# Kernel optimization log

Measured on AMD Instinct MI355X. Metric: run time of the kernel, lower is better.

The kernel has to match this reference:

```python
import jax, jax.numpy as jnp
import numpy as np

FPS_NUM = 8
GROUP_NUM = 512
RADIUS = 0.2
H = 128
OUT = 128
NUM_LAYERS = 4
EPS = 1e-5
BIG = 1e10


def layernorm(x, g, b):
    m = x.mean(-1, keepdims=True)
    v = ((x - m) ** 2).mean(-1, keepdims=True)
    return (x - m) / jnp.sqrt(v + EPS) * g + b


def fps(xyz):
    # sequential farthest point sampling; deterministic start at index 0
    B, N, _ = xyz.shape

    def step(carry, _):
        distance, far = carry
        c = jnp.take_along_axis(xyz, far[:, None, None], axis=1)  # [B,1,3]
        d = jnp.sum((xyz - c) ** 2, axis=-1)                       # [B,N]
        distance = jnp.minimum(distance, d)
        return (distance, jnp.argmax(distance, axis=1)), far

    init = (jnp.full((B, N), BIG, xyz.dtype), jnp.zeros((B,), jnp.int32))
    _, cents = jax.lax.scan(step, init, None, length=FPS_NUM)
    return jnp.transpose(cents)  # [B, FPS_NUM]


def preprocess(xyz):
    B, N, _ = xyz.shape
    cents = fps(xyz)                                               # [B,K]
    cxyz = jnp.take_along_axis(xyz, cents[..., None], axis=1)      # [B,K,3]
    # ball query: pairwise sq-dist, mask outside radius, take GROUP_NUM nearest
    dist = jnp.sum((xyz[:, None, :, :] - cxyz[:, :, None, :]) ** 2, axis=-1)  # [B,K,N]
    dist = jnp.where(dist > RADIUS ** 2, BIG, dist)
    idx = jnp.argsort(dist, axis=-1)[:, :, :GROUP_NUM]             # [B,K,G]
    K = cents.shape[1]
    xyz_exp = jnp.broadcast_to(xyz[:, None, :, :], (B, K, N, 3))
    idx3 = jnp.broadcast_to(idx[..., None], (B, K, GROUP_NUM, 3))
    grouped = jnp.take_along_axis(xyz_exp, idx3, axis=2)           # [B,K,G,3]
    rel = grouped - cxyz[:, :, None, :]
    combined = jnp.concatenate([cxyz[:, :, None, :], rel], axis=2)  # [B,K,G+1,3]
    return combined, cxyz


def setup_inputs() -> dict:
    key = jax.random.key(0)
    ks = jax.random.split(key, 32)
    B, N = 32, 65536
    s = 0.05
    inp = {
        "x": jax.random.normal(ks[0], (B, N, 3), jnp.float32),
        "conv_in_w": jax.random.normal(ks[1], (H, 3), jnp.float32) * s,
        "conv_in_b": jnp.zeros((H,), jnp.float32),
        "layer_w": jax.random.normal(ks[2], (NUM_LAYERS, H, H), jnp.float32) * s,
        "layer_b": jnp.zeros((NUM_LAYERS, H), jnp.float32),
        "glayer_w": jax.random.normal(ks[3], (NUM_LAYERS, H, 2 * H), jnp.float32) * s,
        "glayer_b": jnp.zeros((NUM_LAYERS, H), jnp.float32),
        "conv_out_w": jax.random.normal(ks[4], (OUT, H * NUM_LAYERS), jnp.float32) * s,
        "conv_out_b": jnp.zeros((OUT,), jnp.float32),
        "mlp_w0": jax.random.normal(ks[5], (64, 3), jnp.float32) * s,
        "mlp_b0": jnp.zeros((64,), jnp.float32),
        "ln0_g": jnp.ones((64,), jnp.float32),
        "ln0_b": jnp.zeros((64,), jnp.float32),
        "mlp_w1": jax.random.normal(ks[6], (128, 64), jnp.float32) * s,
        "mlp_b1": jnp.zeros((128,), jnp.float32),
        "ln1_g": jnp.ones((128,), jnp.float32),
        "ln1_b": jnp.zeros((128,), jnp.float32),
        "mlp_w2": jax.random.normal(ks[7], (256, 128), jnp.float32) * s,
        "mlp_b2": jnp.zeros((256,), jnp.float32),
        "ln2_g": jnp.ones((256,), jnp.float32),
        "ln2_b": jnp.zeros((256,), jnp.float32),
        "fp_w": jax.random.normal(ks[8], (OUT, 256), jnp.float32) * s,
        "fp_b": jnp.zeros((OUT,), jnp.float32),
        "fp_ln_g": jnp.ones((OUT,), jnp.float32),
        "fp_ln_b": jnp.zeros((OUT,), jnp.float32),
    }
    return inp


def reference(x, conv_in_w, conv_in_b, layer_w, layer_b, glayer_w, glayer_b,
              conv_out_w, conv_out_b, mlp_w0, mlp_b0, ln0_g, ln0_b,
              mlp_w1, mlp_b1, ln1_g, ln1_b, mlp_w2, mlp_b2, ln2_g, ln2_b,
              fp_w, fp_b, fp_ln_g, fp_ln_b):
    combined, cx = preprocess(x)
    B, K, n, _ = combined.shape
    gp = combined.reshape(B * K, n, 3)
    # conv1x1 stack (LeakyReLU slope 0.0 == ReLU); layout [BK, n, C]
    y = jax.nn.relu(gp @ conv_in_w.T + conv_in_b)
    feats = []
    for i in range(NUM_LAYERS):
        y = jax.nn.relu(y @ layer_w[i].T + layer_b[i])
        yg = y.max(axis=1, keepdims=True)
        y = jnp.concatenate([y, jnp.broadcast_to(yg, y.shape)], axis=-1)
        y = jax.nn.relu(y @ glayer_w[i].T + glayer_b[i])
        feats.append(y)
    y = jnp.concatenate(feats, axis=-1)                 # [BK, n, H*L]
    y = (y @ conv_out_w.T + conv_out_b).max(axis=1)     # [BK, OUT]
    y_global = y.reshape(B, K, -1).max(axis=1)          # [B, OUT]

    c = jax.nn.relu(layernorm(cx @ mlp_w0.T + mlp_b0, ln0_g, ln0_b))
    c = jax.nn.relu(layernorm(c @ mlp_w1.T + mlp_b1, ln1_g, ln1_b))
    c = jax.nn.relu(layernorm(c @ mlp_w2.T + mlp_b2, ln2_g, ln2_b))
    c = c.max(axis=1)                                   # [B, 256]
    cf = layernorm(c @ fp_w.T + fp_b, fp_ln_g, fp_ln_b)  # [B, OUT]
    return (y_global, cf)
```

## Files before the change

kernel.cpp:

```cpp
#include <hip/hip_runtime.h>
#include <cstdint>
#include <cstddef>

#define N_PTS 65536
#define B_SZ 32
#define K_FPS 8
#define GRP 512
#define NP 513
#define HD 128
#define R2C 0.04f
#define BIGF 1e10f

typedef unsigned int u32;
typedef unsigned long long u64;
using bf8  = __attribute__((ext_vector_type(8))) short;
using f32x4 = __attribute__((ext_vector_type(4))) float;

__device__ __forceinline__ unsigned short f2bf(float f) {
  u32 u = __float_as_uint(f);
  u32 r = (u + 0x7FFFu + ((u >> 16) & 1u)) >> 16;
  return (unsigned short)r;
}
__device__ __forceinline__ float bf2f(unsigned short h) {
  return __uint_as_float(((u32)h) << 16);
}
__device__ __forceinline__ u32 xf(float v) {
  u32 u = __float_as_uint(v);
  return (u & 0x80000000u) ? ~u : (u | 0x80000000u);
}
__device__ __forceinline__ float xinv(u32 u) {
  return (u & 0x80000000u) ? __uint_as_float(u & 0x7FFFFFFFu) : __uint_as_float(~u);
}
__device__ __forceinline__ f32x4 mfma16(bf8 a, bf8 b, f32x4 c) {
  return __builtin_amdgcn_mfma_f32_16x16x32_bf16(a, b, c, 0, 0, 0);
}

__global__ void init_all_kernel(u32* __restrict__ slots32,
                                u32* __restrict__ tmaxU,
                                u32* __restrict__ goutU,
                                u32* __restrict__ cmaxU) {
  int i = blockIdx.x * blockDim.x + threadIdx.x;
  if (i < 448) slots32[i] = 0u;
  if (i < 4 * 256 * HD) tmaxU[i] = 0u;
  if (i < 256 * HD) goutU[i] = 0x00800000u;
  if (i < B_SZ * 256) cmaxU[i] = 0u;
}

template <int IT>
__global__ __launch_bounds__(256) void fps_step(const float* __restrict__ x,
                                                u64* __restrict__ slots) {
  int blk = blockIdx.x;
  int b = blk >> 6, s = blk & 63;
  int tid = threadIdx.x;
  const float* xb = x + (size_t)b * N_PTS * 3;
  __shared__ float cx[8], cy[8], cz[8];
  if (tid <= IT) {
    int ci = (tid == 0) ? 0 : (int)(0xFFFFFFFFu - (u32)slots[(tid - 1) * B_SZ + b]);
    cx[tid] = xb[ci * 3 + 0];
    cy[tid] = xb[ci * 3 + 1];
    cz[tid] = xb[ci * 3 + 2];
  }
  __syncthreads();
  float best = -1.0f; int bi = 0;
  int base = s * 1024;
#pragma unroll
  for (int j = 0; j < 4; ++j) {
    int i = base + j * 256 + tid;
    float px = xb[i * 3 + 0], py = xb[i * 3 + 1], pz = xb[i * 3 + 2];
    float d = BIGF;
#pragma unroll
    for (int c = 0; c <= IT; ++c) {
      float dx = px - cx[c], dy = py - cy[c], dz = pz - cz[c];
      d = fminf(d, dx * dx + dy * dy + dz * dz);
    }
    if (d > best) { best = d; bi = i; }
  }
  for (int off = 32; off > 0; off >>= 1) {
    float ov = __shfl_down(best, off);
    int oi = __shfl_down(bi, off);
    if (ov > best || (ov == best && oi < bi)) { best = ov; bi = oi; }
  }
  __shared__ float wv[4]; __shared__ int wi[4];
  if ((tid & 63) == 0) { wv[tid >> 6] = best; wi[tid >> 6] = bi; }
  __syncthreads();
  if (tid == 0) {
    float bv = wv[0]; int bx = wi[0];
    for (int k = 1; k < 4; ++k)
      if (wv[k] > bv || (wv[k] == bv && wi[k] < bx)) { bv = wv[k]; bx = wi[k]; }
    u64 key = ((u64)xf(bv) << 32) | (u64)(0xFFFFFFFFu - (u32)bx);
    atomicMax(&slots[IT * B_SZ + b], key);
  }
}

__global__ __launch_bounds__(1024) void ballq_kernel(const float* __restrict__ x,
                                                     const u64* __restrict__ slots,
                                                     float* __restrict__ cxyz,
                                                     float* __restrict__ grouped) {
  int i0 = blockIdx.x;
  int xcd = i0 & 7, j0 = i0 >> 3;
  int b = xcd + 8 * (j0 >> 3);
  int k = j0 & 7;
  int g = b * 8 + k;
  int tid = threadIdx.x;
  const float* xb = x + (size_t)b * N_PTS * 3;
  __shared__ int sPref[1024];
  __shared__ int s_in[GRP];
  __shared__ int s_out[GRP];
  __shared__ float sc[3];
  if (tid == 0) {
    int ci = (k == 0) ? 0 : (int)(0xFFFFFFFFu - (u32)slots[(k - 1) * B_SZ + b]);
    sc[0] = xb[ci * 3 + 0]; sc[1] = xb[ci * 3 + 1]; sc[2] = xb[ci * 3 + 2];
  }
  __syncthreads();
  float c0 = sc[0], c1 = sc[1], c2 = sc[2];
  int base = tid * 64;
  unsigned long long bm = 0ull;
  int cnt = 0;
  for (int j = 0; j < 64; ++j) {
    int i = base + j;
    float dx = xb[i * 3 + 0] - c0;
    float dy = xb[i * 3 + 1] - c1;
    float dz = xb[i * 3 + 2] - c2;
    float d = dx * dx + dy * dy + dz * dz;
    bool inr = !(d > R2C);
    if (inr) { bm |= (1ull << j); ++cnt; }
  }
  sPref[tid] = cnt;
  __syncthreads();
  for (int off = 1; off < 1024; off <<= 1) {
    int add = (tid >= off) ? sPref[tid - off] : 0;
    __syncthreads();
    sPref[tid] += add;
    __syncthreads();
  }
  int inc = sPref[tid];
  int exc = inc - cnt;
  int outExc = base - exc;
  {
    int ii = exc, oo = outExc;
    for (int j = 0; j < 64; ++j) {
      if ((bm >> j) & 1ull) { if (ii < GRP) s_in[ii] = base + j; ++ii; }
      else                  { if (oo < GRP) s_out[oo] = base + j; ++oo; }
    }
  }
  __syncthreads();
  int incnt = min(sPref[1023], GRP);
  if (tid == 0) {
    cxyz[g * 3 + 0] = c0; cxyz[g * 3 + 1] = c1; cxyz[g * 3 + 2] = c2;
    float* o0 = grouped + (size_t)g * NP * 3;
    o0[0] = c0; o0[1] = c1; o0[2] = c2;
  } else if (tid <= GRP) {
    int j = tid - 1;
    int src = (j < incnt) ? s_in[j] : s_out[j - incnt];
    float* o = grouped + ((size_t)g * NP + 1 + j) * 3;
    o[0] = xb[src * 3 + 0] - c0;
    o[1] = xb[src * 3 + 1] - c1;
    o[2] = xb[src * 3 + 2] - c2;
  }
}

__global__ void wprep_kernel(const float* __restrict__ layer_w,
                             const float* __restrict__ glayer_w,
                             const float* __restrict__ conv_out_w,
                             short* __restrict__ w1h, short* __restrict__ w1l,
                             short* __restrict__ w2h, short* __restrict__ w2l,
                             short* __restrict__ coh, short* __restrict__ col_) {
  int id = blockIdx.x * blockDim.x + threadIdx.x;
  float v; short *dh, *dl; size_t dpos;
  if (id < 65536) {
    int l = id >> 14, o = (id >> 7) & 127, k = id & 127;
    v = layer_w[(size_t)l * 16384 + o * 128 + k];
    dpos = (size_t)l * 16384 + o * 128 + (k ^ ((o & 7) << 3));
    dh = w1h; dl = w1l;
  } else if (id < 131072) {
    int t = id - 65536;
    int l = t >> 14, o = (t >> 7) & 127, k = t & 127;
    v = glayer_w[(size_t)l * 32768 + o * 256 + k];
    dpos = (size_t)l * 16384 + o * 128 + (k ^ ((o & 7) << 3));
    dh = w2h; dl = w2l;
  } else if (id < 196608) {
    int t = id - 131072;
    int o = t >> 9, k = t & 511;
    v = conv_out_w[(size_t)o * 512 + k];
    dpos = (size_t)o * 512 + (k ^ ((o & 7) << 3));
    dh = coh; dl = col_;
  } else return;
  unsigned short h = f2bf(v);
  dh[dpos] = (short)h;
  dl[dpos] = (short)f2bf(v - bf2f(h));
}

__global__ void conv_in_kernel(const float* __restrict__ gp,
                               const float* __restrict__ W,
                               const float* __restrict__ bias,
                               short* __restrict__ oh, short* __restrict__ ol,
                               int M, int Mp) {
  int idx = blockIdx.x * blockDim.x + threadIdx.x;
  if (idx >= Mp * HD) return;
  int r = idx >> 7, c = idx & 127;
  float v = 0.0f;
  if (r < M) {
    const float* p = gp + (size_t)r * 3;
    v = bias[c] + p[0] * W[c * 3 + 0] + p[1] * W[c * 3 + 1] + p[2] * W[c * 3 + 2];
    v = fmaxf(v, 0.0f);
  }
  unsigned short h = f2bf(v);
  size_t pos = (size_t)r * HD + (c ^ ((r & 7) << 3));
  oh[pos] = (short)h;
  ol[pos] = (short)f2bf(v - bf2f(h));
}

template <int MODE>
__global__ __launch_bounds__(256, 2) void mfgemm(
    const short* __restrict__ a0h, const short* __restrict__ a0l,
    const short* __restrict__ a1h, const short* __restrict__ a1l,
    const short* __restrict__ a2h, const short* __restrict__ a2l,
    const short* __restrict__ a3h, const short* __restrict__ a3l,
    const short* __restrict__ wh, const short* __restrict__ wl,
    int wRowShorts,
    const float* __restrict__ bias,
    short* __restrict__ oh, short* __restrict__ ol,
    u32* __restrict__ redU,
    int M) {
  __shared__ short lds[4][128][64];
  const int tid = threadIdx.x;
  const int lane = tid & 63, w = tid >> 6;
  const int wr = w >> 1, wc = w & 1;
  const int m0 = blockIdx.x * 128;
  const int wRB = wRowShorts * 2;

  f32x4 acc[4][4];
#pragma unroll
  for (int i = 0; i < 4; ++i)
#pragma unroll
    for (int j = 0; j < 4; ++j) acc[i][j] = (f32x4){0.f, 0.f, 0.f, 0.f};

  const int NH = (MODE == 2) ? 8 : 2;
  const short* ahp[4] = {a0h, a1h, a2h, a3h};
  const short* alp[4] = {a0l, a1l, a2l, a3l};

#pragma unroll
  for (int hf = 0; hf < NH; ++hf) {
    {
      const char* pAh = (const char*)ahp[hf >> 1] + (size_t)m0 * 256 + (hf & 1) * 128;
      const char* pAl = (const char*)alp[hf >> 1] + (size_t)m0 * 256 + (hf & 1) * 128;
      const char* pWh = (const char*)wh + hf * 128;
      const char* pWl = (const char*)wl + hf * 128;
#pragma unroll
      for (int i = 0; i < 16; ++i) {
        int c2 = i * 256 + tid;
        int plane = c2 >> 10;
        int idx = c2 & 1023;
        int row = idx >> 3, ch = idx & 7;
        const char* s = (plane == 0) ? pAh : (plane == 1) ? pAl
                       : (plane == 2) ? pWh : pWl;
        int rb = (plane < 2) ? 256 : wRB;
        const char* src = s + (size_t)row * rb + ch * 16;
        void* dst = (char*)lds + (size_t)c2 * 16;
        __builtin_amdgcn_global_load_lds(
            (const __attribute__((address_space(1))) u32*)src,
            (__attribute__((address_space(3))) u32*)dst, 16, 0, 0);
      }
    }
    __syncthreads();
#pragma unroll
    for (int kk = 0; kk < 2; ++kk) {
      int k0 = kk * 32 + (lane >> 4) * 8;
      bf8 afh[4], afl[4], bfh[4], bfl[4];
#pragma unroll
      for (int rt = 0; rt < 4; ++rt) {
        int row = wr * 64 + rt * 16 + (lane & 15);
        int kp = k0 ^ ((row & 7) << 3);
        afh[rt] = *(const bf8*)&lds[0][row][kp];
        afl[rt] = *(const bf8*)&lds[1][row][kp];
      }
#pragma unroll
      for (int ct = 0; ct < 4; ++ct) {
        int orow = wc * 64 + ct * 16 + (lane & 15);
        int kp = k0 ^ ((orow & 7) << 3);
        bfh[ct] = *(const bf8*)&lds[2][orow][kp];
        bfl[ct] = *(const bf8*)&lds[3][orow][kp];
      }
#pragma unroll
      for (int rt = 0; rt < 4; ++rt)
#pragma unroll
        for (int ct = 0; ct < 4; ++ct) {
          acc[rt][ct] = mfma16(afh[rt], bfh[ct], acc[rt][ct]);
          acc[rt][ct] = mfma16(afh[rt], bfl[ct], acc[rt][ct]);
          acc[rt][ct] = mfma16(afl[rt], bfh[ct], acc[rt][ct]);
        }
    }
    if (hf + 1 < NH) __syncthreads();
  }

#pragma unroll
  for (int ct = 0; ct < 4; ++ct) {
    int col = wc * 64 + ct * 16 + (lane & 15);
    int curGrp = -1;
    u32 curKey = 0;
#pragma unroll
    for (int rt = 0; rt < 4; ++rt) {
      int rbase = m0 + wr * 64 + rt * 16 + ((lane >> 4) << 2);
#pragma unroll
      for (int reg = 0; reg < 4; ++reg) {
        int row = rbase + reg;
        float v = acc[rt][ct][reg];
        if (MODE == 0) v += bias[col];
        if (MODE == 1) v += bias[(row / 513) * HD + col];
        if (MODE != 2) {
          v = fmaxf(v, 0.0f);
          unsigned short h = f2bf(v);
          unsigned short l2 = f2bf(v - bf2f(h));
          size_t pos = (size_t)row * HD + (col ^ ((row & 7) << 3));
          oh[pos] = (short)h;
          ol[pos] = (short)l2;
        }
        if (MODE == 0 || MODE == 2) {
          if (row < M) {
            int gg = row / 513;
            u32 key = xf(v);
            if (gg != curGrp) {
              if (curGrp >= 0) atomicMax(&redU[curGrp * HD + col], curKey);
              curGrp = gg; curKey = key;
            } else {
              curKey = max(curKey, key);
            }
          }
        }
      }
    }
    if ((MODE == 0 || MODE == 2) && curGrp >= 0)
      atomicMax(&redU[curGrp * HD + col], curKey);
  }
}

__global__ void gvec_kernel(const u32* __restrict__ tmaxU, const float* __restrict__ gw,
                            const float* __restrict__ gb, float* __restrict__ gvec) {
  int g = blockIdx.x, c = threadIdx.x;
  __shared__ float sm[HD];
  sm[c] = xinv(tmaxU[g * HD + c]);
  __syncthreads();
  const float* wr = gw + (size_t)c * (2 * HD) + HD;
  float s = gb[c];
  for (int j = 0; j < HD; ++j) s += sm[j] * wr[j];
  gvec[g * HD + c] = s;
}

__global__ void batchmax_kernel(const u32* __restrict__ goutU,
                                const float* __restrict__ bout,
                                float* __restrict__ out) {
  int b = blockIdx.x, c = threadIdx.x;
  float m = -3.4e38f;
  for (int k = 0; k < K_FPS; ++k) m = fmaxf(m, xinv(goutU[(size_t)(b * K_FPS + k) * HD + c]));
  out[b * HD + c] = m + bout[c];
}

__device__ __forceinline__ void block_ln(float* h, int n, const float* __restrict__ gam,
                                         const float* __restrict__ bet, float* red,
                                         int tid, bool relu) {
  float v = (tid < n) ? h[tid] : 0.0f;
  red[tid] = v;
  __syncthreads();
  for (int s = 128; s > 0; s >>= 1) { if (tid < s) red[tid] += red[tid + s]; __syncthreads(); }
  float mean = red[0] / n;
  __syncthreads();
  float d = (tid < n) ? (h[tid] - mean) : 0.0f;
  red[tid] = d * d;
  __syncthreads();
  for (int s = 128; s > 0; s >>= 1) { if (tid < s) red[tid] += red[tid + s]; __syncthreads(); }
  float var = red[0] / n;
  __syncthreads();
  if (tid < n) {
    float o = (h[tid] - mean) / sqrtf(var + 1e-5f) * gam[tid] + bet[tid];
    if (relu) o = fmaxf(o, 0.0f);
    h[tid] = o;
  }
  __syncthreads();
}

__global__ __launch_bounds__(256) void cpathA_kernel(const float* __restrict__ cxyz,
    const float* __restrict__ w0, const float* __restrict__ b0,
    const float* __restrict__ g0, const float* __restrict__ e0,
    const float* __restrict__ w1, const float* __restrict__ b1,
    const float* __restrict__ g1, const float* __restrict__ e1,
    const float* __restrict__ w2, const float* __restrict__ b2,
    const float* __restrict__ g2, const float* __restrict__ e2,
    u32* __restrict__ cmaxU) {
  int g = blockIdx.x, b = g >> 3, tid = threadIdx.x;
  __shared__ float h[256];
  __shared__ float hb[256];
  __shared__ float red[256];
  const float* cp = cxyz + (size_t)g * 3;
  float p0 = cp[0], p1 = cp[1], p2 = cp[2];
  if (tid < 64)
    h[tid] = b0[tid] + p0 * w0[tid * 3 + 0] + p1 * w0[tid * 3 + 1] + p2 * w0[tid * 3 + 2];
  __syncthreads();
  block_ln(h, 64, g0, e0, red, tid, true);
  if (tid < 128) {
    float s = b1[tid];
    const float* wr = w1 + (size_t)tid * 64;
    for (int j = 0; j < 64; ++j) s += h[j] * wr[j];
    hb[tid] = s;
  }
  __syncthreads();
  block_ln(hb, 128, g1, e1, red, tid, true);
  {
    float s = b2[tid];
    const float* wr = w2 + (size_t)tid * 128;
    for (int j = 0; j < 128; ++j) s += hb[j] * wr[j];
    __syncthreads();
    h[tid] = s;
  }
  __syncthreads();
  block_ln(h, 256, g2, e2, red, tid, true);
  atomicMax(&cmaxU[b * 256 + tid], xf(h[tid]));
}

__global__ __launch_bounds__(256) void cpathB_kernel(const u32* __restrict__ cmaxU,
    const float* __restrict__ fw, const float* __restrict__ fb,
    const float* __restrict__ fg, const float* __restrict__ fe,
    float* __restrict__ out) {
  int b = blockIdx.x, tid = threadIdx.x;
  __shared__ float cm[256];
  __shared__ float h[256];
  __shared__ float red[256];
  cm[tid] = xinv(cmaxU[b * 256 + tid]);
  __syncthreads();
  if (tid < 128) {
    float s = fb[tid];
    const float* wr = fw + (size_t)tid * 256;
    for (int j = 0; j < 256; ++j) s += cm[j] * wr[j];
    h[tid] = s;
  }
  __syncthreads();
  block_ln(h, 128, fg, fe, red, tid, false);
  if (tid < 128) out[b * HD + tid] = h[tid];
}

extern "C" void kernel_launch(void* const* d_in, const int* in_sizes, int n_in,
                              void* d_out, int out_size, void* d_ws, size_t ws_size,
                              hipStream_t stream) {
  (void)in_sizes; (void)n_in; (void)out_size;
  const float* x          = (const float*)d_in[0];
  const float* conv_in_w  = (const float*)d_in[1];
  const float* conv_in_b  = (const float*)d_in[2];
  const float* layer_w    = (const float*)d_in[3];
  const float* layer_b    = (const float*)d_in[4];
  const float* glayer_w   = (const float*)d_in[5];
  const float* glayer_b   = (const float*)d_in[6];
  const float* conv_out_w = (const float*)d_in[7];
  const float* conv_out_b = (const float*)d_in[8];
  const float* mlp_w0 = (const float*)d_in[9];
  const float* mlp_b0 = (const float*)d_in[10];
  const float* ln0_g  = (const float*)d_in[11];
  const float* ln0_b  = (const float*)d_in[12];
  const float* mlp_w1 = (const float*)d_in[13];
  const float* mlp_b1 = (const float*)d_in[14];
  const float* ln1_g  = (const float*)d_in[15];
  const float* ln1_b  = (const float*)d_in[16];
  const float* mlp_w2 = (const float*)d_in[17];
  const float* mlp_b2 = (const float*)d_in[18];
  const float* ln2_g  = (const float*)d_in[19];
  const float* ln2_b  = (const float*)d_in[20];
  const float* fp_w   = (const float*)d_in[21];
  const float* fp_b   = (const float*)d_in[22];
  const float* fp_ln_g = (const float*)d_in[23];
  const float* fp_ln_b = (const float*)d_in[24];

  char* ws = (char*)d_ws;
  size_t off = 0;
  auto carve = [&](size_t bytes) -> void* {
    void* p = ws + off;
    off += (bytes + 255) & ~(size_t)255;
    return p;
  };
  u64* slots   = (u64*)carve(7 * B_SZ * 8);
  float* cxyz  = (float*)carve(256 * 3 * 4);
  float* grouped = (float*)carve((size_t)256 * NP * 3 * 4);
  u32* goutU   = (u32*)carve(256 * HD * 4);
  u32* tmaxU   = (u32*)carve(4 * 256 * HD * 4);
  float* gvec  = (float*)carve(257 * HD * 4);
  u32* cmaxU   = (u32*)carve(B_SZ * 256 * 4);
  short* w1h = (short*)carve(4 * 16384 * 2);
  short* w1l = (short*)carve(4 * 16384 * 2);
  short* w2h = (short*)carve(4 * 16384 * 2);
  short* w2l = (short*)carve(4 * 16384 * 2);
  short* coh = (short*)carve(65536 * 2);
  short* col_ = (short*)carve(65536 * 2);
  size_t fixed = off;

  int C = 8;
  const int cands[5] = {128, 64, 32, 16, 8};
  for (int ci = 0; ci < 5; ++ci) {
    int Cc = cands[ci];
    size_t Mp = ((size_t)(513 * Cc + 127) / 128) * 128;
    size_t need = fixed + 12 * ((Mp * HD * 2 + 255) & ~(size_t)255) + 65536;
    if (need <= ws_size) { C = Cc; break; }
  }
  int Mp = (int)(((size_t)(513 * C + 127) / 128) * 128);
  size_t planeB = (size_t)Mp * HD * 2;
  short* y0h = (short*)carve(planeB); short* y0l = (short*)carve(planeB);
  short* th  = (short*)carve(planeB); short* tl  = (short*)carve(planeB);
  short* fh[4]; short* fl[4];
  for (int l = 0; l < 4; ++l) { fh[l] = (short*)carve(planeB); fl[l] = (short*)carve(planeB); }

  init_all_kernel<<<(4 * 256 * HD + 255) / 256, 256, 0, stream>>>(
      (u32*)slots, tmaxU, goutU, cmaxU);

  fps_step<0><<<2048, 256, 0, stream>>>(x, slots);
  fps_step<1><<<2048, 256, 0, stream>>>(x, slots);
  fps_step<2><<<2048, 256, 0, stream>>>(x, slots);
  fps_step<3><<<2048, 256, 0, stream>>>(x, slots);
  fps_step<4><<<2048, 256, 0, stream>>>(x, slots);
  fps_step<5><<<2048, 256, 0, stream>>>(x, slots);
  fps_step<6><<<2048, 256, 0, stream>>>(x, slots);

  ballq_kernel<<<256, 1024, 0, stream>>>(x, slots, cxyz, grouped);
  wprep_kernel<<<768, 256, 0, stream>>>(layer_w, glayer_w, conv_out_w,
                                        w1h, w1l, w2h, w2l, coh, col_);

  int M = C * 513;
  int nb = Mp / 128;
  for (int g0 = 0; g0 < 256; g0 += C) {
    conv_in_kernel<<<(Mp * HD + 255) / 256, 256, 0, stream>>>(
        grouped + (size_t)g0 * NP * 3, conv_in_w, conv_in_b, y0h, y0l, M, Mp);
    const short* inH = y0h; const short* inL = y0l;
    for (int l = 0; l < 4; ++l) {
      u32* tmaxL = tmaxU + (size_t)l * 256 * HD + (size_t)g0 * HD;
      mfgemm<0><<<nb, 256, 0, stream>>>(
          inH, inL, inH, inL, inH, inL, inH, inL,
          w1h + (size_t)l * 16384, w1l + (size_t)l * 16384, 128,
          layer_b + l * HD, th, tl, tmaxL, M);
      gvec_kernel<<<C, HD, 0, stream>>>(tmaxL, glayer_w + (size_t)l * HD * 2 * HD,
                                        glayer_b + l * HD, gvec);
      mfgemm<1><<<nb, 256, 0, stream>>>(
          th, tl, th, tl, th, tl, th, tl,
          w2h + (size_t)l * 16384, w2l + (size_t)l * 16384, 128,
          gvec, fh[l], fl[l], nullptr, M);
      inH = fh[l]; inL = fl[l];
    }
    mfgemm<2><<<nb, 256, 0, stream>>>(
        fh[0], fl[0], fh[1], fl[1], fh[2], fl[2], fh[3], fl[3],
        coh, col_, 512, nullptr, nullptr, nullptr, goutU + (size_t)g0 * HD, M);
  }
  batchmax_kernel<<<B_SZ, HD, 0, stream>>>(goutU, conv_out_b, (float*)d_out);
  cpathA_kernel<<<256, 256, 0, stream>>>(cxyz,
      mlp_w0, mlp_b0, ln0_g, ln0_b,
      mlp_w1, mlp_b1, ln1_g, ln1_b,
      mlp_w2, mlp_b2, ln2_g, ln2_b, cmaxU);
  cpathB_kernel<<<B_SZ, 256, 0, stream>>>(cmaxU, fp_w, fp_b, fp_ln_g, fp_ln_b,
                                          (float*)d_out + B_SZ * HD);
}
```

Before: 886.5 us.

## Fuse conv_in into first GEMM, halve GEMM tile rows, stage stores via LDS

Removes the separate conv_in kernel by computing the 3->128 input conv inside a new GEMM mode that writes the A tile straight into LDS. This drops the y0 buffers and one full write/read of the activation planes. The GEMM M-tile shrinks from 128 to 64 rows, with occupancy raised to 3 blocks per CU, and outputs are staged through LDS for coalesced 16-byte stores. The block-to-batch mapping in the FPS and ball-query kernels is also remapped for XCD locality. The smaller tile means less weight reuse per block, and the ballq remap changes which batch each block handles.

Result: faster. 779.2 us (-12.1%).

```diff
diff --git a/kernel.cpp b/kernel.cpp
--- a/kernel.cpp
+++ b/kernel.cpp
@@ -13,8 +13,10 @@
 
 typedef unsigned int u32;
 typedef unsigned long long u64;
-using bf8  = __attribute__((ext_vector_type(8))) short;
+using bf8   = __attribute__((ext_vector_type(8))) short;
+using s8v   = __attribute__((ext_vector_type(8))) short;
 using f32x4 = __attribute__((ext_vector_type(4))) float;
+using i32x4 = __attribute__((ext_vector_type(4))) int;
 
 __device__ __forceinline__ unsigned short f2bf(float f) {
   u32 u = __float_as_uint(f);
@@ -49,8 +51,8 @@
 template <int IT>
 __global__ __launch_bounds__(256) void fps_step(const float* __restrict__ x,
                                                 u64* __restrict__ slots) {
-  int blk = blockIdx.x;
-  int b = blk >> 6, s = blk & 63;
+  int p = (blockIdx.x & 7) * 256 + (blockIdx.x >> 3);
+  int b = p >> 6, s = p & 63;
   int tid = threadIdx.x;
   const float* xb = x + (size_t)b * N_PTS * 3;
   __shared__ float cx[8], cy[8], cz[8];
@@ -96,9 +98,9 @@
                                                      const u64* __restrict__ slots,
                                                      float* __restrict__ cxyz,
                                                      float* __restrict__ grouped) {
-  int i0 = blockIdx.x;
-  int xcd = i0 & 7, j0 = i0 >> 3;
-  int b = xcd + 8 * (j0 >> 3);
+  int blk = blockIdx.x;
+  int xcd = blk & 7, j0 = blk >> 3;
+  int b = xcd * 4 + (j0 >> 3);
   int k = j0 & 7;
   int g = b * 8 + k;
   int tid = threadIdx.x;
@@ -190,28 +192,8 @@
   dl[dpos] = (short)f2bf(v - bf2f(h));
 }
 
-__global__ void conv_in_kernel(const float* __restrict__ gp,
-                               const float* __restrict__ W,
-                               const float* __restrict__ bias,
-                               short* __restrict__ oh, short* __restrict__ ol,
-                               int M, int Mp) {
-  int idx = blockIdx.x * blockDim.x + threadIdx.x;
-  if (idx >= Mp * HD) return;
-  int r = idx >> 7, c = idx & 127;
-  float v = 0.0f;
-  if (r < M) {
-    const float* p = gp + (size_t)r * 3;
-    v = bias[c] + p[0] * W[c * 3 + 0] + p[1] * W[c * 3 + 1] + p[2] * W[c * 3 + 2];
-    v = fmaxf(v, 0.0f);
-  }
-  unsigned short h = f2bf(v);
-  size_t pos = (size_t)r * HD + (c ^ ((r & 7) << 3));
-  oh[pos] = (short)h;
-  ol[pos] = (short)f2bf(v - bf2f(h));
-}
-
 template <int MODE>
-__global__ __launch_bounds__(256, 2) void mfgemm(
+__global__ __launch_bounds__(256, 3) void mfgemm(
     const short* __restrict__ a0h, const short* __restrict__ a0l,
     const short* __restrict__ a1h, const short* __restrict__ a1l,
     const short* __restrict__ a2h, const short* __restrict__ a2l,
@@ -219,19 +201,21 @@
     const short* __restrict__ wh, const short* __restrict__ wl,
     int wRowShorts,
     const float* __restrict__ bias,
+    const float* __restrict__ cw, const float* __restrict__ cb,
+    const float* __restrict__ gp,
     short* __restrict__ oh, short* __restrict__ ol,
-    u32* __restrict__ redU,
-    int M) {
-  __shared__ short lds[4][128][64];
+    u32* __restrict__ redU, int M) {
+  __shared__ alignas(16) short ldsA[2][64][64];
+  __shared__ alignas(16) short ldsW[2][128][64];
   const int tid = threadIdx.x;
   const int lane = tid & 63, w = tid >> 6;
   const int wr = w >> 1, wc = w & 1;
-  const int m0 = blockIdx.x * 128;
+  const int m0 = blockIdx.x * 64;
   const int wRB = wRowShorts * 2;
 
-  f32x4 acc[4][4];
-#pragma unroll
-  for (int i = 0; i < 4; ++i)
+  f32x4 acc[2][4];
+#pragma unroll
+  for (int i = 0; i < 2; ++i)
 #pragma unroll
     for (int j = 0; j < 4; ++j) acc[i][j] = (f32x4){0.f, 0.f, 0.f, 0.f};
 
@@ -239,50 +223,91 @@
   const short* ahp[4] = {a0h, a1h, a2h, a3h};
   const short* alp[4] = {a0l, a1l, a2l, a3l};
 
-#pragma unroll
+  float gx = 0.f, gy = 0.f, gz = 0.f;
+  if (MODE == 3) {
+    int row = m0 + (tid >> 2);
+    if (row < M) { gx = gp[row * 3]; gy = gp[row * 3 + 1]; gz = gp[row * 3 + 2]; }
+  }
+
   for (int hf = 0; hf < NH; ++hf) {
-    {
-      const char* pAh = (const char*)ahp[hf >> 1] + (size_t)m0 * 256 + (hf & 1) * 128;
-      const char* pAl = (const char*)alp[hf >> 1] + (size_t)m0 * 256 + (hf & 1) * 128;
-      const char* pWh = (const char*)wh + hf * 128;
-      const char* pWl = (const char*)wl + hf * 128;
-#pragma unroll
-      for (int i = 0; i < 16; ++i) {
+    if (MODE == 3) {
+#pragma unroll
+      for (int i = 0; i < 8; ++i) {
         int c2 = i * 256 + tid;
-        int plane = c2 >> 10;
-        int idx = c2 & 1023;
+        int plane = c2 >> 10, idx = c2 & 1023;
         int row = idx >> 3, ch = idx & 7;
-        const char* s = (plane == 0) ? pAh : (plane == 1) ? pAl
-                       : (plane == 2) ? pWh : pWl;
-        int rb = (plane < 2) ? 256 : wRB;
-        const char* src = s + (size_t)row * rb + ch * 16;
-        void* dst = (char*)lds + (size_t)c2 * 16;
+        const char* s = plane ? (const char*)wl : (const char*)wh;
+        const char* src = s + (size_t)row * wRB + hf * 128 + ch * 16;
+        void* dst = (char*)ldsW[plane] + (size_t)idx * 16;
         __builtin_amdgcn_global_load_lds(
             (const __attribute__((address_space(1))) u32*)src,
             (__attribute__((address_space(3))) u32*)dst, 16, 0, 0);
       }
+      int r = tid >> 2, q = tid & 3;
+      bool real = (m0 + r) < M;
+#pragma unroll
+      for (int jj = 0; jj < 2; ++jj) {
+        short hbuf[8], lbuf[8];
+#pragma unroll
+        for (int j = 0; j < 8; ++j) {
+          int c = hf * 64 + q * 16 + jj * 8 + j;
+          float v = 0.f;
+          if (real)
+            v = fmaxf(cb[c] + gx * cw[c * 3] + gy * cw[c * 3 + 1] + gz * cw[c * 3 + 2], 0.f);
+          unsigned short hh = f2bf(v);
+          hbuf[j] = (short)hh;
+          lbuf[j] = (short)f2bf(v - bf2f(hh));
+        }
+        int pos = (q * 16 + jj * 8) ^ ((r & 7) << 3);
+        *(s8v*)&ldsA[0][r][pos] = *(const s8v*)hbuf;
+        *(s8v*)&ldsA[1][r][pos] = *(const s8v*)lbuf;
+      }
+    } else {
+#pragma unroll
+      for (int i = 0; i < 12; ++i) {
+        int c2 = i * 256 + tid;
+        const char* src;
+        void* dst;
+        if (c2 < 1024) {
+          int plane = c2 >> 9, idx = c2 & 511;
+          int row = idx >> 3, ch = idx & 7;
+          const char* s = plane ? (const char*)alp[hf >> 1] : (const char*)ahp[hf >> 1];
+          src = s + (size_t)(m0 + row) * 256 + (hf & 1) * 128 + ch * 16;
+          dst = (char*)ldsA[plane] + (size_t)idx * 16;
+        } else {
+          int t = c2 - 1024;
+          int plane = t >> 10, idx = t & 1023;
+          int row = idx >> 3, ch = idx & 7;
+          const char* s = plane ? (const char*)wl : (const char*)wh;
+          src = s + (size_t)row * wRB + hf * 128 + ch * 16;
+          dst = (char*)ldsW[plane] + (size_t)idx * 16;
+        }
+        __builtin_amdgcn_global_load_lds(
+            (const __attribute__((address_space(1))) u32*)src,
+            (__attribute__((address_space(3))) u32*)dst, 16, 0, 0);
+      }
     }
     __syncthreads();
 #pragma unroll
     for (int kk = 0; kk < 2; ++kk) {
       int k0 = kk * 32 + (lane >> 4) * 8;
-      bf8 afh[4], afl[4], bfh[4], bfl[4];
-#pragma unroll
-      for (int rt = 0; rt < 4; ++rt) {
-        int row = wr * 64 + rt * 16 + (lane & 15);
+      bf8 afh[2], afl[2], bfh[4], bfl[4];
+#pragma unroll
+      for (int rt = 0; rt < 2; ++rt) {
+        int row = wr * 32 + rt * 16 + (lane & 15);
         int kp = k0 ^ ((row & 7) << 3);
-        afh[rt] = *(const bf8*)&lds[0][row][kp];
-        afl[rt] = *(const bf8*)&lds[1][row][kp];
+        afh[rt] = *(const bf8*)&ldsA[0][row][kp];
+        afl[rt] = *(const bf8*)&ldsA[1][row][kp];
       }
 #pragma unroll
       for (int ct = 0; ct < 4; ++ct) {
         int orow = wc * 64 + ct * 16 + (lane & 15);
         int kp = k0 ^ ((orow & 7) << 3);
-        bfh[ct] = *(const bf8*)&lds[2][orow][kp];
-        bfl[ct] = *(const bf8*)&lds[3][orow][kp];
+        bfh[ct] = *(const bf8*)&ldsW[0][orow][kp];
+        bfl[ct] = *(const bf8*)&ldsW[1][orow][kp];
       }
 #pragma unroll
-      for (int rt = 0; rt < 4; ++rt)
+      for (int rt = 0; rt < 2; ++rt)
 #pragma unroll
         for (int ct = 0; ct < 4; ++ct) {
           acc[rt][ct] = mfma16(afh[rt], bfh[ct], acc[rt][ct]);
@@ -290,47 +315,59 @@
           acc[rt][ct] = mfma16(afl[rt], bfh[ct], acc[rt][ct]);
         }
     }
-    if (hf + 1 < NH) __syncthreads();
-  }
-
+    __syncthreads();
+  }
+
+  constexpr bool DO_STORE = (MODE != 2);
+  constexpr bool DO_RED   = (MODE != 1);
+  short* imgH = (short*)ldsA;
+  short* imgL = (short*)ldsW;
 #pragma unroll
   for (int ct = 0; ct < 4; ++ct) {
     int col = wc * 64 + ct * 16 + (lane & 15);
     int curGrp = -1;
     u32 curKey = 0;
 #pragma unroll
-    for (int rt = 0; rt < 4; ++rt) {
-      int rbase = m0 + wr * 64 + rt * 16 + ((lane >> 4) << 2);
+    for (int rt = 0; rt < 2; ++rt) {
+      int rb = wr * 32 + rt * 16 + ((lane >> 4) << 2);
 #pragma unroll
       for (int reg = 0; reg < 4; ++reg) {
-        int row = rbase + reg;
+        int lrow = rb + reg;
+        int row = m0 + lrow;
         float v = acc[rt][ct][reg];
-        if (MODE == 0) v += bias[col];
+        if (MODE == 0 || MODE == 3) v += bias[col];
         if (MODE == 1) v += bias[(row / 513) * HD + col];
-        if (MODE != 2) {
-          v = fmaxf(v, 0.0f);
-          unsigned short h = f2bf(v);
-          unsigned short l2 = f2bf(v - bf2f(h));
-          size_t pos = (size_t)row * HD + (col ^ ((row & 7) << 3));
-          oh[pos] = (short)h;
-          ol[pos] = (short)l2;
+        if (MODE != 2) v = fmaxf(v, 0.0f);
+        if (DO_STORE) {
+          unsigned short hh = f2bf(v);
+          int pos = lrow * 128 + (col ^ ((lrow & 7) << 3));
+          imgH[pos] = (short)hh;
+          imgL[pos] = (short)f2bf(v - bf2f(hh));
         }
-        if (MODE == 0 || MODE == 2) {
-          if (row < M) {
-            int gg = row / 513;
-            u32 key = xf(v);
-            if (gg != curGrp) {
-              if (curGrp >= 0) atomicMax(&redU[curGrp * HD + col], curKey);
-              curGrp = gg; curKey = key;
-            } else {
-              curKey = max(curKey, key);
-            }
+        if (DO_RED && row < M) {
+          int gg = row / 513;
+          u32 key = xf(v);
+          if (gg != curGrp) {
+            if (curGrp >= 0) atomicMax(&redU[curGrp * HD + col], curKey);
+            curGrp = gg; curKey = key;
+          } else {
+            curKey = max(curKey, key);
           }
         }
       }
     }
-    if ((MODE == 0 || MODE == 2) && curGrp >= 0)
-      atomicMax(&redU[curGrp * HD + col], curKey);
+    if (DO_RED && curGrp >= 0) atomicMax(&redU[curGrp * HD + col], curKey);
+  }
+  if (DO_STORE) {
+    __syncthreads();
+    char* dH = (char*)oh + (size_t)m0 * 256;
+    char* dL = (char*)ol + (size_t)m0 * 256;
+#pragma unroll
+    for (int i = 0; i < 4; ++i) {
+      int idx = i * 256 + tid;
+      *(i32x4*)(dH + (size_t)idx * 16) = *(const i32x4*)((const char*)imgH + (size_t)idx * 16);
+      *(i32x4*)(dL + (size_t)idx * 16) = *(const i32x4*)((const char*)imgL + (size_t)idx * 16);
+    }
   }
 }
 
@@ -493,14 +530,15 @@
   const int cands[5] = {128, 64, 32, 16, 8};
   for (int ci = 0; ci < 5; ++ci) {
     int Cc = cands[ci];
-    size_t Mp = ((size_t)(513 * Cc + 127) / 128) * 128;
-    size_t need = fixed + 12 * ((Mp * HD * 2 + 255) & ~(size_t)255) + 65536;
+    size_t Mp = ((size_t)(513 * Cc + 63) / 64) * 64;
+    size_t need = fixed + 10 * ((Mp * HD * 2 + 255) & ~(size_t)255) + 65536;
     if (need <= ws_size) { C = Cc; break; }
   }
-  int Mp = (int)(((size_t)(513 * C + 127) / 128) * 128);
+  int M = C * 513;
+  int Mp = (int)(((size_t)(M + 63) / 64) * 64);
+  int nb = Mp / 64;
   size_t planeB = (size_t)Mp * HD * 2;
-  short* y0h = (short*)carve(planeB); short* y0l = (short*)carve(planeB);
-  short* th  = (short*)carve(planeB); short* tl  = (short*)carve(planeB);
+  short* th = (short*)carve(planeB); short* tl = (short*)carve(planeB);
   short* fh[4]; short* fl[4];
   for (int l = 0; l < 4; ++l) { fh[l] = (short*)carve(planeB); fl[l] = (short*)carve(planeB); }
 
@@ -519,29 +557,37 @@
   wprep_kernel<<<768, 256, 0, stream>>>(layer_w, glayer_w, conv_out_w,
                                         w1h, w1l, w2h, w2l, coh, col_);
 
-  int M = C * 513;
-  int nb = Mp / 128;
   for (int g0 = 0; g0 < 256; g0 += C) {
-    conv_in_kernel<<<(Mp * HD + 255) / 256, 256, 0, stream>>>(
-        grouped + (size_t)g0 * NP * 3, conv_in_w, conv_in_b, y0h, y0l, M, Mp);
-    const short* inH = y0h; const short* inL = y0l;
-    for (int l = 0; l < 4; ++l) {
+    u32* tmax0 = tmaxU + (size_t)0 * 256 * HD + (size_t)g0 * HD;
+    mfgemm<3><<<nb, 256, 0, stream>>>(
+        nullptr, nullptr, nullptr, nullptr, nullptr, nullptr, nullptr, nullptr,
+        w1h, w1l, 128, layer_b,
+        conv_in_w, conv_in_b, grouped + (size_t)g0 * NP * 3,
+        th, tl, tmax0, M);
+    gvec_kernel<<<C, HD, 0, stream>>>(tmax0, glayer_w, glayer_b, gvec);
+    mfgemm<1><<<nb, 256, 0, stream>>>(
+        th, tl, th, tl, th, tl, th, tl,
+        w2h, w2l, 128, gvec, nullptr, nullptr, nullptr,
+        fh[0], fl[0], nullptr, M);
+    for (int l = 1; l < 4; ++l) {
       u32* tmaxL = tmaxU + (size_t)l * 256 * HD + (size_t)g0 * HD;
       mfgemm<0><<<nb, 256, 0, stream>>>(
-          inH, inL, inH, inL, inH, inL, inH, inL,
+          fh[l-1], fl[l-1], fh[l-1], fl[l-1], fh[l-1], fl[l-1], fh[l-1], fl[l-1],
           w1h + (size_t)l * 16384, w1l + (size_t)l * 16384, 128,
-          layer_b + l * HD, th, tl, tmaxL, M);
+          layer_b + l * HD, nullptr, nullptr, nullptr,
+          th, tl, tmaxL, M);
       gvec_kernel<<<C, HD, 0, stream>>>(tmaxL, glayer_w + (size_t)l * HD * 2 * HD,
                                         glayer_b + l * HD, gvec);
       mfgemm<1><<<nb, 256, 0, stream>>>(
           th, tl, th, tl, th, tl, th, tl,
           w2h + (size_t)l * 16384, w2l + (size_t)l * 16384, 128,
-          gvec, fh[l], fl[l], nullptr, M);
-      inH = fh[l]; inL = fl[l];
+          gvec, nullptr, nullptr, nullptr,
+          fh[l], fl[l], nullptr, M);
     }
     mfgemm<2><<<nb, 256, 0, stream>>>(
         fh[0], fl[0], fh[1], fl[1], fh[2], fl[2], fh[3], fl[3],
-        coh, col_, 512, nullptr, nullptr, nullptr, goutU + (size_t)g0 * HD, M);
+        coh, col_, 512, nullptr, nullptr, nullptr, nullptr,
+        nullptr, nullptr, goutU + (size_t)g0 * HD, M);
   }
   batchmax_kernel<<<B_SZ, HD, 0, stream>>>(goutU, conv_out_b, (float*)d_out);
   cpathA_kernel<<<256, 256, 0, stream>>>(cxyz,
```
